# Performance work log

Hardware: AMD Instinct MI355X
Metric: run time of the kernel (lower is better)

Reference implementation:

```python
import jax, jax.numpy as jnp
import numpy as np
import math

N = 20000; T = 60; D = 158
G = 8           # num_groups
E = 16          # num_experts_per_group
H = 4           # num_heads (of inner-group attention)
DH = E // H     # head_dim = 4
GE = G * E      # hidden_dim = 128
TOP_K = 2


def setup_inputs() -> dict:
    key = jax.random.key(0)
    ks = jax.random.split(key, 12)
    s_in = 1.0 / math.sqrt(T * D)
    s_h = 1.0 / math.sqrt(GE)
    s_e = 1.0 / math.sqrt(E)
    return {
        "x":  jax.random.normal(ks[0], (N, T, D), jnp.float32),
        # router: Linear(T*D -> GE)
        "Wr": jax.random.uniform(ks[1], (T * D, GE), jnp.float32, -s_in, s_in),
        "br": jax.random.uniform(ks[2], (GE,), jnp.float32, -s_in, s_in),
        # experts: per (group, expert) Linear(GE -> 1); weight stored [G, E, GE]
        "We": jax.random.uniform(ks[3], (G, E, GE), jnp.float32, -s_h, s_h),
        "be": jax.random.uniform(ks[4], (G, E), jnp.float32, -s_h, s_h),
        # inner-group attention: per-group Linear(E -> E), torch layout [out, in]
        "Wq": jax.random.uniform(ks[5], (G, E, E), jnp.float32, -s_e, s_e),
        "bq": jax.random.uniform(ks[6], (G, E), jnp.float32, -s_e, s_e),
        "Wk": jax.random.uniform(ks[7], (G, E, E), jnp.float32, -s_e, s_e),
        "bk": jax.random.uniform(ks[8], (G, E), jnp.float32, -s_e, s_e),
        "Wv": jax.random.uniform(ks[9], (G, E, E), jnp.float32, -s_e, s_e),
        "bv": jax.random.uniform(ks[10], (G, E), jnp.float32, -s_e, s_e),
        "Wo": jax.random.uniform(ks[11], (G, E, E), jnp.float32, -s_e, s_e),
        "bo": jnp.zeros((G, E), jnp.float32),
    }


def reference(x, Wr, br, We, be, Wq, bq, Wk, bk, Wv, bv, Wo, bo):
    n = x.shape[0]
    # router: [N, T*D] -> [N, GE]
    h = x.reshape(n, T * D) @ Wr + br
    # top-k gating over the flat GE dim
    _, idx = jax.lax.top_k(h, TOP_K)                       # [N, K]
    mask = jnp.zeros_like(h).at[jnp.arange(n)[:, None], idx].set(1.0)
    masked = jnp.where(mask == 0, -jnp.inf, h)
    rw = jax.nn.softmax(masked, axis=1)                    # [N, GE]
    # all experts as one batched matvec: [N, G, E]
    eo = jnp.einsum('nh,geh->nge', h, We) + be
    # per-group attention (faithful to torch view/transpose: head_dim is the seq axis)
    def proj(W, b):
        y = jnp.einsum('nge,gfe->ngf', eo, W) + b          # [N, G, E]
        return y.reshape(n, G, H, DH).transpose(0, 1, 3, 2)  # [N, G, DH, H]
    Qh, Kh, Vh = proj(Wq, bq), proj(Wk, bk), proj(Wv, bv)
    scores = jnp.einsum('ngdh,ngeh->ngde', Qh, Kh) / math.sqrt(DH)  # [N,G,DH,DH]
    attn = jax.nn.softmax(scores, axis=-1)
    att = jnp.einsum('ngde,ngeh->ngdh', attn, Vh)          # [N, G, DH, H]
    att = att.transpose(0, 1, 3, 2).reshape(n, G, E)       # [N, G, E]
    out = jnp.einsum('nge,gfe->ngf', att, Wo) + bo         # [N, G, E]
    all_out = out.reshape(n, GE)
    predictions = jnp.sum(all_out * rw, axis=1)            # [N]
    return predictions
```

## Files before the change

### kernel.cpp

```cpp
#include <hip/hip_runtime.h>
#include <hip/hip_bf16.h>
#include <math.h>

#define NROWS 20000
#define KDIM  9480
#define GEDIM 128
#define GNUM  8
#define ENUM  16

#define BM 128
#define BK 32
#define NTHREADS 256

__global__ __launch_bounds__(NTHREADS, 2) void router_gemm(
    const float* __restrict__ x, const float* __restrict__ Wr,
    float* __restrict__ partial, int iters_per_chunk)
{
    __shared__ float sA[BM][BK + 4];
    __shared__ float sB[BK][GEDIM];

    const int tid = threadIdx.x;
    const int m0 = blockIdx.x * BM;
    const int s  = blockIdx.y;
    const int kstart = s * iters_per_chunk * BK;
    const int kend   = min(kstart + iters_per_chunk * BK, KDIM);

    const int tr = tid >> 4;
    const int tc = tid & 15;
    const int r0 = tr * 8;
    const int c0 = tc * 4;

    float acc[8][8];
#pragma unroll
    for (int i = 0; i < 8; ++i)
#pragma unroll
        for (int j = 0; j < 8; ++j) acc[i][j] = 0.f;

    for (int k0 = kstart; k0 < kend; k0 += BK) {
#pragma unroll
        for (int i = 0; i < 4; ++i) {
            int fid = tid + i * NTHREADS;
            int r   = fid >> 3;
            int c4  = fid & 7;
            int grow = m0 + r;
            int gk   = k0 + c4 * 4;
            float4 v = make_float4(0.f, 0.f, 0.f, 0.f);
            if (grow < NROWS && gk < kend)
                v = *(const float4*)(x + (size_t)grow * KDIM + gk);
            *(float4*)&sA[r][c4 * 4] = v;
        }
#pragma unroll
        for (int i = 0; i < 4; ++i) {
            int fid = tid + i * NTHREADS;
            int kk  = fid >> 5;
            int c4  = fid & 31;
            int gk  = k0 + kk;
            float4 v = make_float4(0.f, 0.f, 0.f, 0.f);
            if (gk < kend)
                v = *(const float4*)(Wr + (size_t)gk * GEDIM + c4 * 4);
            *(float4*)&sB[kk][c4 * 4] = v;
        }
        __syncthreads();

        float chunk[8][8];
#pragma unroll
        for (int i = 0; i < 8; ++i)
#pragma unroll
            for (int j = 0; j < 8; ++j) chunk[i][j] = 0.f;

#pragma unroll
        for (int kq = 0; kq < BK / 4; ++kq) {
            float4 a[8];
#pragma unroll
            for (int i = 0; i < 8; ++i)
                a[i] = *(const float4*)&sA[r0 + i][kq * 4];
#pragma unroll
            for (int j = 0; j < 4; ++j) {
                int kk = kq * 4 + j;
                float4 b0 = *(const float4*)&sB[kk][c0];
                float4 b1 = *(const float4*)&sB[kk][c0 + 64];
#pragma unroll
                for (int i = 0; i < 8; ++i) {
                    float av = (j == 0) ? a[i].x : (j == 1) ? a[i].y
                             : (j == 2) ? a[i].z : a[i].w;
                    chunk[i][0] += av * b0.x;
                    chunk[i][1] += av * b0.y;
                    chunk[i][2] += av * b0.z;
                    chunk[i][3] += av * b0.w;
                    chunk[i][4] += av * b1.x;
                    chunk[i][5] += av * b1.y;
                    chunk[i][6] += av * b1.z;
                    chunk[i][7] += av * b1.w;
                }
            }
        }
#pragma unroll
        for (int i = 0; i < 8; ++i)
#pragma unroll
            for (int j = 0; j < 8; ++j) acc[i][j] += chunk[i][j];
        __syncthreads();
    }

    float* pbase = partial + (size_t)s * NROWS * GEDIM;
#pragma unroll
    for (int i = 0; i < 8; ++i) {
        int row = m0 + r0 + i;
        if (row < NROWS) {
            float4 v0 = make_float4(acc[i][0], acc[i][1], acc[i][2], acc[i][3]);
            float4 v1 = make_float4(acc[i][4], acc[i][5], acc[i][6], acc[i][7]);
            *(float4*)(pbase + (size_t)row * GEDIM + c0)      = v0;
            *(float4*)(pbase + (size_t)row * GEDIM + c0 + 64) = v1;
        }
    }
}

__global__ __launch_bounds__(64) void tail_kernel(
    const float* __restrict__ partial, int S,
    const float* __restrict__ br,
    const float* __restrict__ We, const float* __restrict__ be,
    const float* __restrict__ Wq, const float* __restrict__ bq,
    const float* __restrict__ Wk, const float* __restrict__ bk,
    const float* __restrict__ Wv, const float* __restrict__ bv,
    const float* __restrict__ Wo, const float* __restrict__ bo,
    float* __restrict__ out)
{
    const int n    = blockIdx.x;
    const int lane = threadIdx.x;

    __shared__ float hbuf[GEDIM];
    __shared__ float eobuf[2][ENUM];
    __shared__ float qbuf[2][ENUM], kbuf[2][ENUM], vbuf[2][ENUM];
    __shared__ float abuf[2][ENUM];
    __shared__ float attbuf[2][ENUM];
    __shared__ float obuf[2];

    float h0 = br[lane];
    float h1 = br[lane + 64];
    for (int s = 0; s < S; ++s) {
        const float* p = partial + ((size_t)s * NROWS + n) * GEDIM;
        h0 += p[lane];
        h1 += p[lane + 64];
    }
    hbuf[lane]      = h0;
    hbuf[lane + 64] = h1;

    float v1, v2; int i1, i2;
    if (h1 > h0) { v1 = h1; i1 = lane + 64; v2 = h0; i2 = lane; }
    else         { v1 = h0; i1 = lane;      v2 = h1; i2 = lane + 64; }
#pragma unroll
    for (int m = 1; m <= 32; m <<= 1) {
        float ov1 = __shfl_xor(v1, m);
        float ov2 = __shfl_xor(v2, m);
        int   oi1 = __shfl_xor(i1, m);
        int   oi2 = __shfl_xor(i2, m);
        bool a_first = (v1 > ov1) || (v1 == ov1 && i1 < oi1);
        float w1v = a_first ? v1  : ov1;  int w1i = a_first ? i1  : oi1;
        float l1v = a_first ? ov1 : v1;   int l1i = a_first ? oi1 : i1;
        float w2v = a_first ? v2  : ov2;  int w2i = a_first ? i2  : oi2;
        bool s_first = (w2v > l1v) || (w2v == l1v && w2i < l1i);
        v1 = w1v; i1 = w1i;
        v2 = s_first ? w2v : l1v;
        i2 = s_first ? w2i : l1i;
    }
    float t  = expf(v2 - v1);
    float wa = 1.0f / (1.0f + t);
    float wb = 1.0f - wa;

    const int ga = i1 >> 4, fa = i1 & 15;
    const int gb = i2 >> 4, fb = i2 & 15;

    __syncthreads();

    {
        int e   = lane & 15;
        int sel = (lane >> 4) & 1;
        int kh  = lane >> 5;
        int g   = sel ? gb : ga;
        const float* w  = We + (size_t)(g * ENUM + e) * GEDIM + kh * 64;
        const float* hp = hbuf + kh * 64;
        float acc = 0.f;
#pragma unroll
        for (int k = 0; k < 64; ++k) acc += hp[k] * w[k];
        acc += __shfl_xor(acc, 32);
        if (kh == 0) eobuf[sel][e] = acc + be[g * ENUM + e];
    }
    __syncthreads();

    if (lane < 32) {
        int f   = lane & 15;
        int sel = lane >> 4;
        int g   = sel ? gb : ga;
        int base = (g * ENUM + f) * ENUM;
        float q = bq[g * ENUM + f];
        float k = bk[g * ENUM + f];
        float v = bv[g * ENUM + f];
#pragma unroll
        for (int e2 = 0; e2 < ENUM; ++e2) {
            float eov = eobuf[sel][e2];
            q += eov * Wq[base + e2];
            k += eov * Wk[base + e2];
            v += eov * Wv[base + e2];
        }
        qbuf[sel][f] = q;
        kbuf[sel][f] = k;
        vbuf[sel][f] = v;
    }
    __syncthreads();

    if (lane < 32) {
        int sel = lane >> 4;
        int d   = (lane >> 2) & 3;
        int e   = lane & 3;
        float sc = 0.f;
#pragma unroll
        for (int hh = 0; hh < 4; ++hh)
            sc += qbuf[sel][hh * 4 + d] * kbuf[sel][hh * 4 + e];
        sc *= 0.5f;
        float mx = fmaxf(sc, __shfl_xor(sc, 1));
        mx = fmaxf(mx, __shfl_xor(mx, 2));
        float p = expf(sc - mx);
        float sum = p + __shfl_xor(p, 1);
        sum += __shfl_xor(sum, 2);
        abuf[sel][d * 4 + e] = p / sum;
    }
    __syncthreads();

    if (lane < 32) {
        int sel = lane >> 4;
        int d   = (lane >> 2) & 3;
        int hh  = lane & 3;
        float a = 0.f;
#pragma unroll
        for (int e2 = 0; e2 < 4; ++e2)
            a += abuf[sel][d * 4 + e2] * vbuf[sel][hh * 4 + e2];
        attbuf[sel][hh * 4 + d] = a;
    }
    __syncthreads();

    if (lane < 2) {
        int sel = lane;
        int g = sel ? gb : ga;
        int f = sel ? fb : fa;
        float o = bo[g * ENUM + f];
        int base = (g * ENUM + f) * ENUM;
#pragma unroll
        for (int e2 = 0; e2 < ENUM; ++e2)
            o += attbuf[sel][e2] * Wo[base + e2];
        obuf[sel] = o;
    }
    __syncthreads();
    if (lane == 0)
        out[n] = wa * obuf[0] + wb * obuf[1];
}

extern "C" void kernel_launch(void* const* d_in, const int* in_sizes, int n_in,
                              void* d_out, int out_size, void* d_ws, size_t ws_size,
                              hipStream_t stream)
{
    const float* x  = (const float*)d_in[0];
    const float* Wr = (const float*)d_in[1];
    const float* br = (const float*)d_in[2];
    const float* We = (const float*)d_in[3];
    const float* be = (const float*)d_in[4];
    const float* Wq = (const float*)d_in[5];
    const float* bq = (const float*)d_in[6];
    const float* Wk = (const float*)d_in[7];
    const float* bk = (const float*)d_in[8];
    const float* Wv = (const float*)d_in[9];
    const float* bv = (const float*)d_in[10];
    const float* Wo = (const float*)d_in[11];
    const float* bo = (const float*)d_in[12];
    float* out = (float*)d_out;
    float* partial = (float*)d_ws;

    const size_t slice = (size_t)NROWS * GEDIM * sizeof(float);
    int S = (int)(ws_size / slice);
    if (S > 8) S = 8;
    if (S < 1) S = 1;

    const int total_iters = (KDIM + BK - 1) / BK;
    const int iters_per_chunk = (total_iters + S - 1) / S;

    dim3 ggrid((NROWS + BM - 1) / BM, S);
    router_gemm<<<ggrid, NTHREADS, 0, stream>>>(x, Wr, partial, iters_per_chunk);

    tail_kernel<<<NROWS, 64, 0, stream>>>(partial, S, br,
                                          We, be, Wq, bq, Wk, bk, Wv, bv, Wo, bo,
                                          out);
}
```

Baseline: 1.660 ms.

## Run router GEMM on bf16 MFMA with three-way split for fp32 accuracy

Replaces the scalar FP32 router GEMM with bf16 MFMA instructions. Both x and Wr are split into high/mid/low bf16 parts, and six cross products are accumulated to approximate fp32 precision. Wr is pre-split and transposed by a new conversion kernel on every call, global loads are register-prefetched one tile ahead, and split-K is capped at 4. The tail kernel now packs four rows per block and uses float4 loads. The cost is six MFMAs per tile plus in-kernel splitting of x, with slightly different rounding behaviour.

Result: faster. 1.570 ms (-5.4%).

```diff
diff --git a/kernel.cpp b/kernel.cpp
--- a/kernel.cpp
+++ b/kernel.cpp
@@ -1,5 +1,4 @@
 #include <hip/hip_runtime.h>
-#include <hip/hip_bf16.h>
 #include <math.h>
 
 #define NROWS 20000
@@ -11,110 +10,196 @@
 #define BM 128
 #define BK 32
 #define NTHREADS 256
+#define WPAD 9504
+#define WRELEM (GEDIM * WPAD)
+#define TROWS 4
+
+using bf16x8 = __attribute__((ext_vector_type(8))) short;
+using f32x4  = __attribute__((ext_vector_type(4))) float;
+
+#define MFMA16(a, b, c) __builtin_amdgcn_mfma_f32_16x16x32_bf16((a), (b), (c), 0, 0, 0)
+
+__device__ __forceinline__ unsigned short bsplit(float f, float& rem) {
+    unsigned u = __float_as_uint(f);
+    unsigned r = u + 0x7fffu + ((u >> 16) & 1u);
+    unsigned short h = (unsigned short)(r >> 16);
+    rem = f - __uint_as_float((unsigned)h << 16);
+    return h;
+}
+
+__device__ __forceinline__ void split3(float f, unsigned short& h,
+                                       unsigned short& m, unsigned short& l) {
+    float r1, r2, r3;
+    h = bsplit(f, r1);
+    m = bsplit(r1, r2);
+    l = bsplit(r2, r3);
+}
+
+__global__ void wr_convert(const float* __restrict__ Wr,
+                           unsigned short* __restrict__ Wh,
+                           unsigned short* __restrict__ Wm,
+                           unsigned short* __restrict__ Wl)
+{
+    __shared__ float tile[128][GEDIM + 4];
+    const int tid = threadIdx.x;
+    const int k0  = blockIdx.x * 128;
+#pragma unroll
+    for (int i = 0; i < 16; ++i) {
+        int fid = tid + i * 256;
+        int kk  = fid >> 5;
+        int c4  = (fid & 31) * 4;
+        float4 v = make_float4(0.f, 0.f, 0.f, 0.f);
+        if (k0 + kk < KDIM)
+            v = *(const float4*)(Wr + (size_t)(k0 + kk) * GEDIM + c4);
+        *(float4*)&tile[kk][c4] = v;
+    }
+    __syncthreads();
+    const int c = tid >> 1, half = tid & 1;
+#pragma unroll
+    for (int j4 = 0; j4 < 16; ++j4) {
+        int kb = half * 64 + j4 * 4;
+        if (k0 + kb >= WPAD) continue;
+        ushort4 hv, mv, lv;
+#pragma unroll
+        for (int jj = 0; jj < 4; ++jj) {
+            float f = tile[kb + jj][c];
+            split3(f, ((unsigned short*)&hv)[jj], ((unsigned short*)&mv)[jj],
+                      ((unsigned short*)&lv)[jj]);
+        }
+        size_t off = (size_t)c * WPAD + (k0 + kb);
+        *(ushort4*)(Wh + off) = hv;
+        *(ushort4*)(Wm + off) = mv;
+        *(ushort4*)(Wl + off) = lv;
+    }
+}
 
 __global__ __launch_bounds__(NTHREADS, 2) void router_gemm(
-    const float* __restrict__ x, const float* __restrict__ Wr,
-    float* __restrict__ partial, int iters_per_chunk)
+    const float* __restrict__ x,
+    const unsigned short* __restrict__ Wh,
+    const unsigned short* __restrict__ Wm,
+    const unsigned short* __restrict__ Wl,
+    float* __restrict__ partial, int ipc)
 {
-    __shared__ float sA[BM][BK + 4];
-    __shared__ float sB[BK][GEDIM];
-
-    const int tid = threadIdx.x;
-    const int m0 = blockIdx.x * BM;
-    const int s  = blockIdx.y;
-    const int kstart = s * iters_per_chunk * BK;
-    const int kend   = min(kstart + iters_per_chunk * BK, KDIM);
-
-    const int tr = tid >> 4;
-    const int tc = tid & 15;
-    const int r0 = tr * 8;
-    const int c0 = tc * 4;
-
-    float acc[8][8];
-#pragma unroll
-    for (int i = 0; i < 8; ++i)
-#pragma unroll
-        for (int j = 0; j < 8; ++j) acc[i][j] = 0.f;
-
-    for (int k0 = kstart; k0 < kend; k0 += BK) {
+    __shared__ __align__(16) unsigned short sXh[BM][BK], sXm[BM][BK], sXl[BM][BK];
+    __shared__ __align__(16) unsigned short sWh[GEDIM][BK], sWm[GEDIM][BK], sWl[GEDIM][BK];
+
+    const int tid  = threadIdx.x;
+    const int lane = tid & 63;
+    const int wid  = tid >> 6;
+    const int wm_  = wid >> 1, wn_ = wid & 1;
+    const int fr   = lane & 15, fq = lane >> 4;
+    const int m0   = blockIdx.x * BM;
+
+    const int kstart = blockIdx.y * ipc * BK;
+    const int kend   = min(kstart + ipc * BK, WPAD);
+
+    f32x4 acc[4][4];
+#pragma unroll
+    for (int i = 0; i < 4; ++i)
+#pragma unroll
+        for (int j = 0; j < 4; ++j) acc[i][j] = f32x4{0.f, 0.f, 0.f, 0.f};
+
+    float4 xr[4];
+    uint4  wr[3][2];
+
+    auto load_tile = [&](int k0) {
 #pragma unroll
         for (int i = 0; i < 4; ++i) {
             int fid = tid + i * NTHREADS;
-            int r   = fid >> 3;
-            int c4  = fid & 7;
-            int grow = m0 + r;
-            int gk   = k0 + c4 * 4;
+            int r = fid >> 3, kc = (fid & 7) * 4;
+            int grow = m0 + r, gk = k0 + kc;
             float4 v = make_float4(0.f, 0.f, 0.f, 0.f);
-            if (grow < NROWS && gk < kend)
+            if (grow < NROWS && gk < KDIM)
                 v = *(const float4*)(x + (size_t)grow * KDIM + gk);
-            *(float4*)&sA[r][c4 * 4] = v;
-        }
+            xr[i] = v;
+        }
+#pragma unroll
+        for (int i = 0; i < 2; ++i) {
+            int fid = tid + i * NTHREADS;
+            int cc = fid >> 2, kq = (fid & 3) * 8;
+            size_t off = (size_t)cc * WPAD + k0 + kq;
+            wr[0][i] = *(const uint4*)(Wh + off);
+            wr[1][i] = *(const uint4*)(Wm + off);
+            wr[2][i] = *(const uint4*)(Wl + off);
+        }
+    };
+
+    load_tile(kstart);
+
+    for (int k0 = kstart; k0 < kend; k0 += BK) {
 #pragma unroll
         for (int i = 0; i < 4; ++i) {
             int fid = tid + i * NTHREADS;
-            int kk  = fid >> 5;
-            int c4  = fid & 31;
-            int gk  = k0 + kk;
-            float4 v = make_float4(0.f, 0.f, 0.f, 0.f);
-            if (gk < kend)
-                v = *(const float4*)(Wr + (size_t)gk * GEDIM + c4 * 4);
-            *(float4*)&sB[kk][c4 * 4] = v;
+            int r = fid >> 3, kc = (fid & 7) * 4;
+            float4 v = xr[i];
+            ushort4 hv, mv, lv;
+            split3(v.x, hv.x, mv.x, lv.x);
+            split3(v.y, hv.y, mv.y, lv.y);
+            split3(v.z, hv.z, mv.z, lv.z);
+            split3(v.w, hv.w, mv.w, lv.w);
+            *(ushort4*)&sXh[r][kc] = hv;
+            *(ushort4*)&sXm[r][kc] = mv;
+            *(ushort4*)&sXl[r][kc] = lv;
+        }
+#pragma unroll
+        for (int i = 0; i < 2; ++i) {
+            int fid = tid + i * NTHREADS;
+            int cc = fid >> 2, kq = (fid & 3) * 8;
+            *(uint4*)&sWh[cc][kq] = wr[0][i];
+            *(uint4*)&sWm[cc][kq] = wr[1][i];
+            *(uint4*)&sWl[cc][kq] = wr[2][i];
         }
         __syncthreads();
 
-        float chunk[8][8];
-#pragma unroll
-        for (int i = 0; i < 8; ++i)
-#pragma unroll
-            for (int j = 0; j < 8; ++j) chunk[i][j] = 0.f;
-
-#pragma unroll
-        for (int kq = 0; kq < BK / 4; ++kq) {
-            float4 a[8];
-#pragma unroll
-            for (int i = 0; i < 8; ++i)
-                a[i] = *(const float4*)&sA[r0 + i][kq * 4];
-#pragma unroll
-            for (int j = 0; j < 4; ++j) {
-                int kk = kq * 4 + j;
-                float4 b0 = *(const float4*)&sB[kk][c0];
-                float4 b1 = *(const float4*)&sB[kk][c0 + 64];
-#pragma unroll
-                for (int i = 0; i < 8; ++i) {
-                    float av = (j == 0) ? a[i].x : (j == 1) ? a[i].y
-                             : (j == 2) ? a[i].z : a[i].w;
-                    chunk[i][0] += av * b0.x;
-                    chunk[i][1] += av * b0.y;
-                    chunk[i][2] += av * b0.z;
-                    chunk[i][3] += av * b0.w;
-                    chunk[i][4] += av * b1.x;
-                    chunk[i][5] += av * b1.y;
-                    chunk[i][6] += av * b1.z;
-                    chunk[i][7] += av * b1.w;
+        if (k0 + BK < kend) load_tile(k0 + BK);
+
+        bf16x8 ah[4], am[4], al[4];
+#pragma unroll
+        for (int mt = 0; mt < 4; ++mt) {
+            int r = wm_ * 64 + mt * 16 + fr;
+            ah[mt] = *(const bf16x8*)&sXh[r][fq * 8];
+            am[mt] = *(const bf16x8*)&sXm[r][fq * 8];
+            al[mt] = *(const bf16x8*)&sXl[r][fq * 8];
+        }
+#pragma unroll
+        for (int nt = 0; nt < 4; ++nt) {
+            int cidx = wn_ * 64 + nt * 16 + fr;
+            bf16x8 bh = *(const bf16x8*)&sWh[cidx][fq * 8];
+            bf16x8 bm = *(const bf16x8*)&sWm[cidx][fq * 8];
+            bf16x8 bl = *(const bf16x8*)&sWl[cidx][fq * 8];
+#pragma unroll
+            for (int mt = 0; mt < 4; ++mt) {
+                f32x4 a = acc[mt][nt];
+                a = MFMA16(ah[mt], bh, a);
+                a = MFMA16(ah[mt], bm, a);
+                a = MFMA16(am[mt], bh, a);
+                a = MFMA16(ah[mt], bl, a);
+                a = MFMA16(al[mt], bh, a);
+                a = MFMA16(am[mt], bm, a);
+                acc[mt][nt] = a;
+            }
+        }
+        __syncthreads();
+    }
+
+    float* pbase = partial + (size_t)blockIdx.y * NROWS * GEDIM;
+#pragma unroll
+    for (int mt = 0; mt < 4; ++mt) {
+#pragma unroll
+        for (int j = 0; j < 4; ++j) {
+            int row = m0 + wm_ * 64 + mt * 16 + fq * 4 + j;
+            if (row < NROWS) {
+#pragma unroll
+                for (int nt = 0; nt < 4; ++nt) {
+                    int col = wn_ * 64 + nt * 16 + fr;
+                    pbase[(size_t)row * GEDIM + col] = acc[mt][nt][j];
                 }
             }
         }
-#pragma unroll
-        for (int i = 0; i < 8; ++i)
-#pragma unroll
-            for (int j = 0; j < 8; ++j) acc[i][j] += chunk[i][j];
-        __syncthreads();
-    }
-
-    float* pbase = partial + (size_t)s * NROWS * GEDIM;
-#pragma unroll
-    for (int i = 0; i < 8; ++i) {
-        int row = m0 + r0 + i;
-        if (row < NROWS) {
-            float4 v0 = make_float4(acc[i][0], acc[i][1], acc[i][2], acc[i][3]);
-            float4 v1 = make_float4(acc[i][4], acc[i][5], acc[i][6], acc[i][7]);
-            *(float4*)(pbase + (size_t)row * GEDIM + c0)      = v0;
-            *(float4*)(pbase + (size_t)row * GEDIM + c0 + 64) = v1;
-        }
-    }
-}
-
-__global__ __launch_bounds__(64) void tail_kernel(
+    }
+}
+
+__global__ __launch_bounds__(256, 4) void tail_kernel(
     const float* __restrict__ partial, int S,
     const float* __restrict__ br,
     const float* __restrict__ We, const float* __restrict__ be,
@@ -124,15 +209,16 @@
     const float* __restrict__ Wo, const float* __restrict__ bo,
     float* __restrict__ out)
 {
-    const int n    = blockIdx.x;
-    const int lane = threadIdx.x;
-
-    __shared__ float hbuf[GEDIM];
-    __shared__ float eobuf[2][ENUM];
-    __shared__ float qbuf[2][ENUM], kbuf[2][ENUM], vbuf[2][ENUM];
-    __shared__ float abuf[2][ENUM];
-    __shared__ float attbuf[2][ENUM];
-    __shared__ float obuf[2];
+    const int w    = threadIdx.x >> 6;
+    const int lane = threadIdx.x & 63;
+    const int n    = blockIdx.x * TROWS + w;
+
+    __shared__ __align__(16) float hbuf[TROWS][GEDIM];
+    __shared__ __align__(16) float eobuf[TROWS][2][ENUM];
+    __shared__ float qbuf[TROWS][2][ENUM], kbuf[TROWS][2][ENUM], vbuf[TROWS][2][ENUM];
+    __shared__ float abuf[TROWS][2][ENUM];
+    __shared__ __align__(16) float attbuf[TROWS][2][ENUM];
+    __shared__ float obuf[TROWS][2];
 
     float h0 = br[lane];
     float h1 = br[lane + 64];
@@ -141,8 +227,8 @@
         h0 += p[lane];
         h1 += p[lane + 64];
     }
-    hbuf[lane]      = h0;
-    hbuf[lane + 64] = h1;
+    hbuf[w][lane]      = h0;
+    hbuf[w][lane + 64] = h1;
 
     float v1, v2; int i1, i2;
     if (h1 > h0) { v1 = h1; i1 = lane + 64; v2 = h0; i2 = lane; }
@@ -172,17 +258,20 @@
     __syncthreads();
 
     {
-        int e   = lane & 15;
-        int sel = (lane >> 4) & 1;
-        int kh  = lane >> 5;
+        int e   = (lane >> 1) & 15;
+        int sel = lane >> 5;
+        int q   = lane & 1;
         int g   = sel ? gb : ga;
-        const float* w  = We + (size_t)(g * ENUM + e) * GEDIM + kh * 64;
-        const float* hp = hbuf + kh * 64;
+        const float4* w4 = (const float4*)(We + (size_t)(g * ENUM + e) * GEDIM + q * 64);
+        const float4* h4 = (const float4*)&hbuf[w][q * 64];
         float acc = 0.f;
 #pragma unroll
-        for (int k = 0; k < 64; ++k) acc += hp[k] * w[k];
-        acc += __shfl_xor(acc, 32);
-        if (kh == 0) eobuf[sel][e] = acc + be[g * ENUM + e];
+        for (int j = 0; j < 16; ++j) {
+            float4 a = w4[j], b = h4[j];
+            acc += a.x * b.x + a.y * b.y + a.z * b.z + a.w * b.w;
+        }
+        acc += __shfl_xor(acc, 1);
+        if (q == 0) eobuf[w][sel][e] = acc + be[g * ENUM + e];
     }
     __syncthreads();
 
@@ -191,19 +280,22 @@
         int sel = lane >> 4;
         int g   = sel ? gb : ga;
         int base = (g * ENUM + f) * ENUM;
+        const float4* q4 = (const float4*)(Wq + base);
+        const float4* k4 = (const float4*)(Wk + base);
+        const float4* v4 = (const float4*)(Wv + base);
         float q = bq[g * ENUM + f];
         float k = bk[g * ENUM + f];
         float v = bv[g * ENUM + f];
 #pragma unroll
-        for (int e2 = 0; e2 < ENUM; ++e2) {
-            float eov = eobuf[sel][e2];
-            q += eov * Wq[base + e2];
-            k += eov * Wk[base + e2];
-            v += eov * Wv[base + e2];
-        }
-        qbuf[sel][f] = q;
-        kbuf[sel][f] = k;
-        vbuf[sel][f] = v;
+        for (int j = 0; j < 4; ++j) {
+            float4 e4 = *(const float4*)&eobuf[w][sel][j * 4];
+            float4 aa = q4[j]; q += e4.x*aa.x + e4.y*aa.y + e4.z*aa.z + e4.w*aa.w;
+            float4 bb = k4[j]; k += e4.x*bb.x + e4.y*bb.y + e4.z*bb.z + e4.w*bb.w;
+            float4 cc = v4[j]; v += e4.x*cc.x + e4.y*cc.y + e4.z*cc.z + e4.w*cc.w;
+        }
+        qbuf[w][sel][f] = q;
+        kbuf[w][sel][f] = k;
+        vbuf[w][sel][f] = v;
     }
     __syncthreads();
 
@@ -214,14 +306,14 @@
         float sc = 0.f;
 #pragma unroll
         for (int hh = 0; hh < 4; ++hh)
-            sc += qbuf[sel][hh * 4 + d] * kbuf[sel][hh * 4 + e];
+            sc += qbuf[w][sel][hh * 4 + d] * kbuf[w][sel][hh * 4 + e];
         sc *= 0.5f;
         float mx = fmaxf(sc, __shfl_xor(sc, 1));
         mx = fmaxf(mx, __shfl_xor(mx, 2));
         float p = expf(sc - mx);
         float sum = p + __shfl_xor(p, 1);
         sum += __shfl_xor(sum, 2);
-        abuf[sel][d * 4 + e] = p / sum;
+        abuf[w][sel][d * 4 + e] = p / sum;
     }
     __syncthreads();
 
@@ -232,8 +324,8 @@
         float a = 0.f;
 #pragma unroll
         for (int e2 = 0; e2 < 4; ++e2)
-            a += abuf[sel][d * 4 + e2] * vbuf[sel][hh * 4 + e2];
-        attbuf[sel][hh * 4 + d] = a;
+            a += abuf[w][sel][d * 4 + e2] * vbuf[w][sel][hh * 4 + e2];
+        attbuf[w][sel][hh * 4 + d] = a;
     }
     __syncthreads();
 
@@ -241,16 +333,20 @@
         int sel = lane;
         int g = sel ? gb : ga;
         int f = sel ? fb : fa;
+        int base = (g * ENUM + f) * ENUM;
+        const float4* o4 = (const float4*)(Wo + base);
         float o = bo[g * ENUM + f];
-        int base = (g * ENUM + f) * ENUM;
-#pragma unroll
-        for (int e2 = 0; e2 < ENUM; ++e2)
-            o += attbuf[sel][e2] * Wo[base + e2];
-        obuf[sel] = o;
+#pragma unroll
+        for (int j = 0; j < 4; ++j) {
+            float4 aa = o4[j];
+            float4 tt = *(const float4*)&attbuf[w][sel][j * 4];
+            o += tt.x*aa.x + tt.y*aa.y + tt.z*aa.z + tt.w*aa.w;
+        }
+        obuf[w][sel] = o;
     }
     __syncthreads();
     if (lane == 0)
-        out[n] = wa * obuf[0] + wb * obuf[1];
+        out[n] = wa * obuf[w][0] + wb * obuf[w][1];
 }
 
 extern "C" void kernel_launch(void* const* d_in, const int* in_sizes, int n_in,
@@ -271,20 +367,26 @@
     const float* Wo = (const float*)d_in[11];
     const float* bo = (const float*)d_in[12];
     float* out = (float*)d_out;
-    float* partial = (float*)d_ws;
+
+    unsigned short* Wh = (unsigned short*)d_ws;
+    unsigned short* Wm = Wh + WRELEM;
+    unsigned short* Wl = Wm + WRELEM;
+    const size_t wr_bytes = (size_t)3 * WRELEM * sizeof(unsigned short);
+    float* partial = (float*)((char*)d_ws + wr_bytes);
 
     const size_t slice = (size_t)NROWS * GEDIM * sizeof(float);
-    int S = (int)(ws_size / slice);
-    if (S > 8) S = 8;
+    int S = (int)((ws_size - wr_bytes) / slice);
+    if (S > 4) S = 4;
     if (S < 1) S = 1;
 
-    const int total_iters = (KDIM + BK - 1) / BK;
-    const int iters_per_chunk = (total_iters + S - 1) / S;
+    const int total_iters = WPAD / BK;
+    const int ipc = (total_iters + S - 1) / S;
+
+    wr_convert<<<dim3((WPAD + 127) / 128), 256, 0, stream>>>(Wr, Wh, Wm, Wl);
 
     dim3 ggrid((NROWS + BM - 1) / BM, S);
-    router_gemm<<<ggrid, NTHREADS, 0, stream>>>(x, Wr, partial, iters_per_chunk);
-
-    tail_kernel<<<NROWS, 64, 0, stream>>>(partial, S, br,
-                                          We, be, Wq, bq, Wk, bk, Wv, bv, Wo, bo,
-                                          out);
-}
+    router_gemm<<<ggrid, NTHREADS, 0, stream>>>(x, Wh, Wm, Wl, partial, ipc);
+
+    tail_kernel<<<NROWS / TROWS, 256, 0, stream>>>(partial, S, br,
+        We, be, Wq, bq, Wk, bk, Wv, bv, Wo, bo, out);
+}
```
